# Kernel optimization log

Hardware: AMD Instinct MI355X
Metric: run time of the kernel (lower is better)

## Reference

```python
import jax, jax.numpy as jnp
import numpy as np

# Sizes (all graphs equal-sized so adaptive pooling is a clean reshape-mean)
G = 256          # number of graphs (batch.max()+1)
N = 2048         # nodes per graph (divisible by POOL)
C = 512          # in_channels
POOL = 32        # pool_size
HID = 64         # hidden_dim
LN_EPS = 1e-5


def setup_inputs() -> dict:
    key = jax.random.key(0)
    ks = jax.random.split(key, 12)
    def u(k, shape, fan_in):
        b = 1.0 / np.sqrt(fan_in)
        return jax.random.uniform(k, shape, jnp.float32, -b, b)
    return {
        "x": jax.random.normal(ks[0], (G * N, C), jnp.float32),
        "batch": jnp.repeat(jnp.arange(G, dtype=jnp.int64), N),
        # Conv1d(in=C, out=HID, k=3), Conv1d(in=HID, out=HID//2, k=3)
        "conv1_w": u(ks[1], (HID, C, 3), C * 3),
        "conv1_b": u(ks[2], (HID,), C * 3),
        "conv2_w": u(ks[3], (HID // 2, HID, 3), HID * 3),
        "conv2_b": u(ks[4], (HID // 2,), HID * 3),
        # fc layers: Linear((HID//2)*POOL -> HID), Linear(HID -> HID)
        "fc1_w": u(ks[5], (HID, (HID // 2) * POOL), (HID // 2) * POOL),
        "fc1_b": u(ks[6], (HID,), (HID // 2) * POOL),
        "fc2_w": u(ks[7], (HID, HID), HID),
        "fc2_b": u(ks[8], (HID,), HID),
        # shared LayerNorm(HID)
        "ln_g": jnp.ones((HID,), jnp.float32),
        "ln_b": jnp.zeros((HID,), jnp.float32),
        # output Linear(HID -> 1)
        "out_w": u(ks[9], (1, HID), HID),
        "out_b": u(ks[10], (1,), HID),
    }


def _conv1d(h, w, b):
    # h: [G, Cin, L], w: [Cout, Cin, 3] -> [G, Cout, L] (padding=1)
    y = jax.lax.conv_general_dilated(h, w, window_strides=(1,), padding='SAME',
                                     dimension_numbers=('NCH', 'OIH', 'NCH'))
    return y + b[None, :, None]


def _layernorm(h, g, b):
    mu = h.mean(-1, keepdims=True)
    var = ((h - mu) ** 2).mean(-1, keepdims=True)
    return (h - mu) * jax.lax.rsqrt(var + LN_EPS) * g + b


def reference(x, batch, conv1_w, conv1_b, conv2_w, conv2_b,
              fc1_w, fc1_b, fc2_w, fc2_b, ln_g, ln_b, out_w, out_b):
    # batch is sorted with equal-sized graphs -> reshape replaces the per-graph loop
    xg = x.reshape(G, N, C)
    # AdaptiveAvgPool1d(POOL): N divisible by POOL -> exact bin mean of size N//POOL
    pooled = xg.reshape(G, POOL, N // POOL, C).mean(axis=2)      # [G, POOL, C]
    h = pooled.transpose(0, 2, 1)                                # [G, C, POOL]
    h = jax.nn.relu(_conv1d(h, conv1_w, conv1_b))                # [G, HID, POOL]
    h = jax.nn.relu(_conv1d(h, conv2_w, conv2_b))                # [G, HID//2, POOL]
    h = h.reshape(G, -1)                                         # [G, (HID//2)*POOL]
    for w, b in ((fc1_w, fc1_b), (fc2_w, fc2_b)):
        h = h @ w.T + b
        h = jax.nn.relu(_layernorm(h, ln_g, ln_b))
    return h @ out_w.T + out_b                                   # [G, 1]
```

## Files before the change

### kernel.cpp

```cpp
#include <hip/hip_runtime.h>
#include <math.h>

#define G_    256
#define N_    2048
#define C_    512
#define POOL_ 32
#define BIN_  64
#define HID_  64
#define HHALF_ 32
#define C4_   128
#define HT_S  36
#define H2_S  36
#define LN_EPS_ 1e-5f

__device__ __forceinline__ float wave_reduce_sum64(float v) {
    #pragma unroll
    for (int m = 1; m < 64; m <<= 1) v += __shfl_xor(v, m, 64);
    return v;
}

__global__ __launch_bounds__(256) void fused_graphnet_kernel(
    const float* __restrict__ x,
    const float* __restrict__ c1w, const float* __restrict__ c1b,
    const float* __restrict__ c2w, const float* __restrict__ c2b,
    const float* __restrict__ f1w, const float* __restrict__ f1b,
    const float* __restrict__ f2w, const float* __restrict__ f2b,
    const float* __restrict__ lng, const float* __restrict__ lnb,
    const float* __restrict__ ow,  const float* __restrict__ ob,
    float* __restrict__ out)
{
    __shared__ __align__(16) float hT[C_ * HT_S];
    __shared__ __align__(16) float h2[HID_ * H2_S];
    __shared__ __align__(16) float f3[HHALF_ * POOL_];
    __shared__ float p4[256];
    __shared__ __align__(16) float aLDS[HID_];

    const int g = blockIdx.x;
    const int t = threadIdx.x;

    {
        const float4* x4 = (const float4*)x;
        const int c4  = t & 127;
        const int prg = t >> 7;
        #pragma unroll 1
        for (int it = 0; it < 16; ++it) {
            const int p = prg + (it << 1);
            const size_t base = ((size_t)g * N_ + (size_t)p * BIN_) * C4_ + c4;
            float sx = 0.f, sy = 0.f, sz = 0.f, sw = 0.f;
            #pragma unroll
            for (int r = 0; r < BIN_; ++r) {
                float4 v = x4[base + (size_t)r * C4_];
                sx += v.x; sy += v.y; sz += v.z; sw += v.w;
            }
            const float inv = 1.0f / 64.0f;
            const int c0 = c4 << 2;
            hT[(c0 + 0) * HT_S + p] = sx * inv;
            hT[(c0 + 1) * HT_S + p] = sy * inv;
            hT[(c0 + 2) * HT_S + p] = sz * inv;
            hT[(c0 + 3) * HT_S + p] = sw * inv;
        }
    }
    __syncthreads();

    {
        const int co    = t & 63;
        const int lbase = (t >> 6) << 3;
        float acc[8];
        #pragma unroll
        for (int i = 0; i < 8; ++i) acc[i] = 0.f;
        const int   off_l = (lbase == 0)  ? lbase : (lbase - 1);
        const float ml    = (lbase == 0)  ? 0.f : 1.f;
        const int   off_r = (lbase == 24) ? lbase : (lbase + 8);
        const float mr    = (lbase == 24) ? 0.f : 1.f;
        const float* wbase = c1w + (size_t)co * (C_ * 3);
        #pragma unroll 2
        for (int cin = 0; cin < C_; ++cin) {
            const float* row = &hT[cin * HT_S];
            const float4 a0 = *(const float4*)&row[lbase];
            const float4 a1 = *(const float4*)&row[lbase + 4];
            float hv[10];
            hv[0] = row[off_l] * ml;
            hv[1] = a0.x; hv[2] = a0.y; hv[3] = a0.z; hv[4] = a0.w;
            hv[5] = a1.x; hv[6] = a1.y; hv[7] = a1.z; hv[8] = a1.w;
            hv[9] = row[off_r] * mr;
            const float* wp = wbase + cin * 3;
            const float w0 = wp[0], w1 = wp[1], w2 = wp[2];
            #pragma unroll
            for (int i = 0; i < 8; ++i)
                acc[i] = fmaf(w0, hv[i], fmaf(w1, hv[i + 1], fmaf(w2, hv[i + 2], acc[i])));
        }
        const float b = c1b[co];
        #pragma unroll
        for (int i = 0; i < 8; ++i)
            h2[co * H2_S + lbase + i] = fmaxf(acc[i] + b, 0.f);
    }
    __syncthreads();

    {
        const int co    = t & 31;
        const int lbase = (t >> 5) << 2;
        float acc[4] = {0.f, 0.f, 0.f, 0.f};
        const int   off_l = (lbase == 0)  ? lbase : (lbase - 1);
        const float ml    = (lbase == 0)  ? 0.f : 1.f;
        const int   off_r = (lbase == 28) ? lbase : (lbase + 4);
        const float mr    = (lbase == 28) ? 0.f : 1.f;
        const float* wbase = c2w + (size_t)co * (HID_ * 3);
        #pragma unroll 4
        for (int cin = 0; cin < HID_; ++cin) {
            const float* row = &h2[cin * H2_S];
            const float4 a0 = *(const float4*)&row[lbase];
            float hv[6];
            hv[0] = row[off_l] * ml;
            hv[1] = a0.x; hv[2] = a0.y; hv[3] = a0.z; hv[4] = a0.w;
            hv[5] = row[off_r] * mr;
            const float* wp = wbase + cin * 3;
            const float w0 = wp[0], w1 = wp[1], w2 = wp[2];
            #pragma unroll
            for (int i = 0; i < 4; ++i)
                acc[i] = fmaf(w0, hv[i], fmaf(w1, hv[i + 1], fmaf(w2, hv[i + 2], acc[i])));
        }
        const float b = c2b[co];
        #pragma unroll
        for (int i = 0; i < 4; ++i)
            f3[co * POOL_ + lbase + i] = fmaxf(acc[i] + b, 0.f);
    }
    __syncthreads();

    {
        const int o = t >> 2, q = t & 3;
        const float4* wrow = (const float4*)(f1w + (size_t)o * 1024 + q * 256);
        const float4* frow = (const float4*)(f3 + q * 256);
        float s = 0.f;
        #pragma unroll
        for (int i = 0; i < 64; ++i) {
            const float4 wv = wrow[i], fv = frow[i];
            s = fmaf(wv.x, fv.x, s); s = fmaf(wv.y, fv.y, s);
            s = fmaf(wv.z, fv.z, s); s = fmaf(wv.w, fv.w, s);
        }
        p4[t] = s;
    }
    __syncthreads();
    if (t < 64) {
        float v = p4[t * 4] + p4[t * 4 + 1] + p4[t * 4 + 2] + p4[t * 4 + 3] + f1b[t];
        const float mu  = wave_reduce_sum64(v) * (1.0f / 64.0f);
        const float d   = v - mu;
        const float var = wave_reduce_sum64(d * d) * (1.0f / 64.0f);
        const float y   = d * rsqrtf(var + LN_EPS_) * lng[t] + lnb[t];
        aLDS[t] = fmaxf(y, 0.f);
    }
    __syncthreads();

    {
        const int o = t >> 2, q = t & 3;
        const float4* wrow = (const float4*)(f2w + (size_t)o * 64 + q * 16);
        float s = 0.f;
        #pragma unroll
        for (int i = 0; i < 4; ++i) {
            const float4 wv = wrow[i];
            const float4 av = *(const float4*)&aLDS[q * 16 + i * 4];
            s = fmaf(wv.x, av.x, s); s = fmaf(wv.y, av.y, s);
            s = fmaf(wv.z, av.z, s); s = fmaf(wv.w, av.w, s);
        }
        p4[t] = s;
    }
    __syncthreads();

    if (t < 64) {
        float v = p4[t * 4] + p4[t * 4 + 1] + p4[t * 4 + 2] + p4[t * 4 + 3] + f2b[t];
        const float mu  = wave_reduce_sum64(v) * (1.0f / 64.0f);
        const float d   = v - mu;
        const float var = wave_reduce_sum64(d * d) * (1.0f / 64.0f);
        const float y   = d * rsqrtf(var + LN_EPS_) * lng[t] + lnb[t];
        const float bb  = fmaxf(y, 0.f);
        const float tot = wave_reduce_sum64(bb * ow[t]);
        if (t == 0) out[g] = tot + ob[0];
    }
}

extern "C" void kernel_launch(void* const* d_in, const int* in_sizes, int n_in,
                              void* d_out, int out_size, void* d_ws, size_t ws_size,
                              hipStream_t stream) {
    const float* x   = (const float*)d_in[0];
    const float* c1w = (const float*)d_in[2];
    const float* c1b = (const float*)d_in[3];
    const float* c2w = (const float*)d_in[4];
    const float* c2b = (const float*)d_in[5];
    const float* f1w = (const float*)d_in[6];
    const float* f1b = (const float*)d_in[7];
    const float* f2w = (const float*)d_in[8];
    const float* f2b = (const float*)d_in[9];
    const float* lng = (const float*)d_in[10];
    const float* lnb = (const float*)d_in[11];
    const float* ow  = (const float*)d_in[12];
    const float* ob  = (const float*)d_in[13];
    float* out = (float*)d_out;

    fused_graphnet_kernel<<<G_, 256, 0, stream>>>(
        x, c1w, c1b, c2w, c2b, f1w, f1b, f2w, f2b, lng, lnb, ow, ob, out);

    (void)in_sizes; (void)n_in; (void)out_size; (void)d_ws; (void)ws_size;
}
```

Before: 260.1 us.

## Split pooling into a high-parallelism kernel separate from the per-graph tail

Moves the adaptive average pooling out of the fused per-graph kernel into its own kernel with one block per (graph, bin), with two half-bins reduced through shared memory. Pooled results go to workspace and a tail kernel runs the convs, FC layers and LayerNorms per graph. The aim is more blocks in flight for the bandwidth-bound read of x. The cost is an extra launch and a workspace write and read.

```diff
diff --git a/kernel.cpp b/kernel.cpp
--- a/kernel.cpp
+++ b/kernel.cpp
@@ -19,8 +19,39 @@
     return v;
 }
 
-__global__ __launch_bounds__(256) void fused_graphnet_kernel(
-    const float* __restrict__ x,
+__global__ __launch_bounds__(256) void pool_kernel(
+    const float* __restrict__ x, float* __restrict__ pooled)
+{
+    __shared__ float4 part[C4_];
+    const int b = blockIdx.x;
+    const int t = threadIdx.x;
+    const int c4   = t & 127;
+    const int half = t >> 7;
+
+    const float4* x4 = (const float4*)x;
+    const size_t base = ((size_t)b * BIN_ + (size_t)half * 32) * C4_ + c4;
+    float sx = 0.f, sy = 0.f, sz = 0.f, sw = 0.f;
+    #pragma unroll
+    for (int r = 0; r < 32; ++r) {
+        float4 v = x4[base + (size_t)r * C4_];
+        sx += v.x; sy += v.y; sz += v.z; sw += v.w;
+    }
+    if (half) part[c4] = make_float4(sx, sy, sz, sw);
+    __syncthreads();
+    if (!half) {
+        const float4 o = part[c4];
+        const float inv = 1.0f / 64.0f;
+        float4 r;
+        r.x = (sx + o.x) * inv;
+        r.y = (sy + o.y) * inv;
+        r.z = (sz + o.z) * inv;
+        r.w = (sw + o.w) * inv;
+        ((float4*)pooled)[(size_t)b * C4_ + c4] = r;
+    }
+}
+
+__global__ __launch_bounds__(256) void tail_kernel(
+    const float* __restrict__ pooled,
     const float* __restrict__ c1w, const float* __restrict__ c1b,
     const float* __restrict__ c2w, const float* __restrict__ c2b,
     const float* __restrict__ f1w, const float* __restrict__ f1b,
@@ -39,25 +70,18 @@
     const int t = threadIdx.x;
 
     {
-        const float4* x4 = (const float4*)x;
-        const int c4  = t & 127;
-        const int prg = t >> 7;
-        #pragma unroll 1
-        for (int it = 0; it < 16; ++it) {
-            const int p = prg + (it << 1);
-            const size_t base = ((size_t)g * N_ + (size_t)p * BIN_) * C4_ + c4;
-            float sx = 0.f, sy = 0.f, sz = 0.f, sw = 0.f;
-            #pragma unroll
-            for (int r = 0; r < BIN_; ++r) {
-                float4 v = x4[base + (size_t)r * C4_];
-                sx += v.x; sy += v.y; sz += v.z; sw += v.w;
-            }
-            const float inv = 1.0f / 64.0f;
+        const float4* p4g = (const float4*)(pooled + (size_t)g * POOL_ * C_);
+        #pragma unroll
+        for (int i = 0; i < 16; ++i) {
+            const int idx = t + i * 256;
+            const int p   = idx >> 7;
+            const int c4  = idx & 127;
+            const float4 v = p4g[idx];
             const int c0 = c4 << 2;
-            hT[(c0 + 0) * HT_S + p] = sx * inv;
-            hT[(c0 + 1) * HT_S + p] = sy * inv;
-            hT[(c0 + 2) * HT_S + p] = sz * inv;
-            hT[(c0 + 3) * HT_S + p] = sw * inv;
+            hT[(c0 + 0) * HT_S + p] = v.x;
+            hT[(c0 + 1) * HT_S + p] = v.y;
+            hT[(c0 + 2) * HT_S + p] = v.z;
+            hT[(c0 + 3) * HT_S + p] = v.w;
         }
     }
     __syncthreads();
@@ -195,8 +219,11 @@
     const float* ob  = (const float*)d_in[13];
     float* out = (float*)d_out;
 
-    fused_graphnet_kernel<<<G_, 256, 0, stream>>>(
-        x, c1w, c1b, c2w, c2b, f1w, f1b, f2w, f2b, lng, lnb, ow, ob, out);
-
-    (void)in_sizes; (void)n_in; (void)out_size; (void)d_ws; (void)ws_size;
-}
+    float* pooled = (float*)d_ws;
+
+    pool_kernel<<<G_ * POOL_, 256, 0, stream>>>(x, pooled);
+    tail_kernel<<<G_, 256, 0, stream>>>(
+        pooled, c1w, c1b, c2w, c2b, f1w, f1b, f2w, f2b, lng, lnb, ow, ob, out);
+
+    (void)in_sizes; (void)n_in; (void)out_size; (void)ws_size;
+}
```

Result: slower. 290.3 us (+11.6%).
